# Kernel tuning notes

Measured on AMD Instinct MI355X. Metric: run time of the kernel, lower is better.

The kernel has to match this reference:

```python
import jax, jax.numpy as jnp
import numpy as np

HEADS = 2
OUT_CH = 128
NEG_SLOPE_ATT = 0.2   # GATv2Conv attention LeakyReLU
NEG_SLOPE_ACT = 0.01  # nn.LeakyReLU default
BN_EPS = 1e-5


def setup_inputs() -> dict:
    key = jax.random.key(0)
    ks = jax.random.split(key, 8)
    B, C, D, H, W = 2, 128, 8, 32, 32
    N = B * D * H * W            # 16384 graph nodes
    E = 196608                   # avg degree 12
    x = jax.random.normal(ks[0], (B, C, D, H, W), dtype=jnp.float32)
    edge_index = jax.random.randint(ks[1], (2, E), 0, N, dtype=jnp.int64)
    lin_w = jax.random.normal(ks[2], (C, HEADS * OUT_CH), dtype=jnp.float32) * (1.0 / np.sqrt(C))
    lin_b = jax.random.normal(ks[3], (HEADS * OUT_CH,), dtype=jnp.float32) * 0.02
    att = jax.random.normal(ks[4], (HEADS, OUT_CH), dtype=jnp.float32) * (1.0 / np.sqrt(OUT_CH))
    gat_bias = jax.random.normal(ks[5], (OUT_CH,), dtype=jnp.float32) * 0.02
    bn_gamma = jnp.ones((OUT_CH,), dtype=jnp.float32)
    bn_beta = jnp.zeros((OUT_CH,), dtype=jnp.float32)
    return {"x": x, "edge_index": edge_index, "lin_w": lin_w, "lin_b": lin_b,
            "att": att, "gat_bias": gat_bias, "bn_gamma": bn_gamma, "bn_beta": bn_beta}


def _gatv2(xf, src, dst, lin_w, lin_b, att, gat_bias, n_nodes):
    # shared-weights GATv2: x' = x W + b, per edge e=(j->i): score = a . lrelu(x'_i + x'_j)
    h = (xf @ lin_w + lin_b).reshape(n_nodes, HEADS, OUT_CH)  # [N, H, C]
    x_src = h[src]                                            # [E, H, C] messages
    logits = jnp.einsum('ehc,hc->eh', jax.nn.leaky_relu(x_src + h[dst], NEG_SLOPE_ATT), att)
    # segment softmax over edges sharing the same target node
    m = jax.ops.segment_max(logits, dst, num_segments=n_nodes)      # [N, H]
    ex = jnp.exp(logits - m[dst])
    denom = jax.ops.segment_sum(ex, dst, num_segments=n_nodes)      # [N, H]
    alpha = ex / denom[dst]
    out = jax.ops.segment_sum(x_src * alpha[..., None], dst, num_segments=n_nodes)  # [N, H, C]
    return out.mean(axis=1) + gat_bias  # concat=False -> head mean


def reference(x, edge_index, lin_w, lin_b, att, gat_bias, bn_gamma, bn_beta):
    B, C, D, H, W = x.shape
    N = B * D * H * W
    xf = x.reshape(B, C, -1).transpose(0, 2, 1).reshape(N, C)
    # add_self_loops=True (PyG default)
    loop = jnp.arange(N, dtype=edge_index.dtype)
    src = jnp.concatenate([edge_index[0], loop])
    dst = jnp.concatenate([edge_index[1], loop])
    out = _gatv2(xf, src, dst, lin_w, lin_b, att, gat_bias, N)      # [N, OUT_CH]
    out = out.reshape(B, D * H * W, OUT_CH).transpose(0, 2, 1).reshape(B, OUT_CH, D, H, W)
    # BatchNorm3d (training-mode batch stats, biased variance)
    mean = out.mean(axis=(0, 2, 3, 4), keepdims=True)
    var = out.var(axis=(0, 2, 3, 4), keepdims=True)
    out = (out - mean) / jnp.sqrt(var + BN_EPS)
    out = out * bn_gamma.reshape(1, -1, 1, 1, 1) + bn_beta.reshape(1, -1, 1, 1, 1)
    return jax.nn.leaky_relu(out, NEG_SLOPE_ACT)
```

## Files before the change

### kernel.cpp

```cpp
#include <hip/hip_runtime.h>
#include <math.h>

#define N_NODES 16384
#define CIN 128
#define HOUT 256
#define OUTC 128
#define NEG_ATT 0.2f
#define NEG_ACT 0.01f
#define BN_EPS 1e-5f

static __device__ __forceinline__ unsigned short f2bf(float f) {
    unsigned int u = __float_as_uint(f);
    unsigned int r = (u + 0x7FFFu + ((u >> 16) & 1u)) >> 16;
    return (unsigned short)r;
}
static __device__ __forceinline__ float bf2f(unsigned short s) {
    return __uint_as_float(((unsigned int)s) << 16);
}

__global__ __launch_bounds__(256) void gemm_kernel(const float* __restrict__ x,
                                                   const float* __restrict__ lin_w,
                                                   const float* __restrict__ lin_b,
                                                   unsigned short* __restrict__ h) {
    __shared__ float As[32][64];
    __shared__ float Bs[32][64];
    const int t = threadIdx.x;
    const int n0 = blockIdx.y * 64;
    const int o0 = blockIdx.x * 64;
    const int b = n0 >> 13;
    const int s0 = n0 & 8191;
    const int tx = t & 15;
    const int ty = t >> 4;
    float acc[4][4] = {};

    const int col = t & 63;
    const int r0 = t >> 6;

    for (int kk = 0; kk < CIN; kk += 32) {
#pragma unroll
        for (int kr = 0; kr < 32; kr += 4) {
            int k = kk + kr + r0;
            As[kr + r0][col] = x[((b * CIN + k) << 13) + s0 + col];
            Bs[kr + r0][col] = lin_w[k * HOUT + o0 + col];
        }
        __syncthreads();
#pragma unroll
        for (int k = 0; k < 32; k++) {
            float4 av = ((const float4*)(&As[k][0]))[ty];
            float4 bv = ((const float4*)(&Bs[k][0]))[tx];
            float a[4] = {av.x, av.y, av.z, av.w};
            float bb[4] = {bv.x, bv.y, bv.z, bv.w};
#pragma unroll
            for (int i = 0; i < 4; i++)
#pragma unroll
                for (int j = 0; j < 4; j++)
                    acc[i][j] = fmaf(a[i], bb[j], acc[i][j]);
        }
        __syncthreads();
    }
    float4 lb = *(const float4*)(&lin_b[o0 + tx * 4]);
#pragma unroll
    for (int i = 0; i < 4; i++) {
        int n = n0 + ty * 4 + i;
        ushort4 o;
        o.x = f2bf(acc[i][0] + lb.x);
        o.y = f2bf(acc[i][1] + lb.y);
        o.z = f2bf(acc[i][2] + lb.z);
        o.w = f2bf(acc[i][3] + lb.w);
        ((ushort4*)h)[n * 64 + (o0 >> 2) + tx] = o;
    }
}

__global__ void count_kernel(const int* __restrict__ dst, int* __restrict__ deg, int E) {
    int e = blockIdx.x * 256 + threadIdx.x;
    if (e < E) atomicAdd(&deg[dst[e]], 1);
}

__global__ __launch_bounds__(1024) void scan_kernel(const int* __restrict__ deg,
                                                    int* __restrict__ row_ptr,
                                                    int* __restrict__ cursor) {
    __shared__ int sums[1024];
    const int t = threadIdx.x;
    int local[16];
    int s = 0;
#pragma unroll
    for (int k = 0; k < 16; k++) {
        local[k] = deg[t * 16 + k];
        s += local[k];
    }
    sums[t] = s;
    __syncthreads();
    for (int off = 1; off < 1024; off <<= 1) {
        int v = (t >= off) ? sums[t - off] : 0;
        __syncthreads();
        sums[t] += v;
        __syncthreads();
    }
    int run = sums[t] - s;
#pragma unroll
    for (int k = 0; k < 16; k++) {
        row_ptr[t * 16 + k] = run;
        cursor[t * 16 + k] = run;
        run += local[k];
    }
    if (t == 1023) row_ptr[N_NODES] = run;
}

__global__ void scatter_kernel(const int* __restrict__ edges, int* __restrict__ cursor,
                               int* __restrict__ csr, int E) {
    int e = blockIdx.x * 256 + threadIdx.x;
    if (e < E) {
        int s = edges[e];
        int d = edges[E + e];
        int p = atomicAdd(&cursor[d], 1);
        csr[p] = s;
    }
}

__global__ __launch_bounds__(256) void gat_kernel(const unsigned short* __restrict__ h,
                                                  const int* __restrict__ row_ptr,
                                                  const int* __restrict__ csr,
                                                  const float* __restrict__ att,
                                                  const float* __restrict__ gat_bias,
                                                  float* __restrict__ gat) {
    const int t = threadIdx.x;
    const int lane = t & 63;
    const int node = (blockIdx.x << 2) + (t >> 6);
    const ushort4* __restrict__ h4 = (const ushort4*)h;

    ushort4 hd4 = h4[(node << 6) + lane];
    float hdx = bf2f(hd4.x), hdy = bf2f(hd4.y), hdz = bf2f(hd4.z), hdw = bf2f(hd4.w);
    float4 a4 = ((const float4*)att)[lane];
    float m = -INFINITY, denom = 0.0f;
    float4 acc = make_float4(0.f, 0.f, 0.f, 0.f);

    const int beg = row_ptr[node];
    const int end = row_ptr[node + 1];
    const int cnt = end - beg + 1;

    for (int base = 0; base < cnt; base += 4) {
        int j[4];
#pragma unroll
        for (int u = 0; u < 4; u++) {
            int e = base + u;
            j[u] = (e == 0 || e >= cnt) ? node : csr[beg + e - 1];
        }
        float4 hj[4];
        float p[4];
#pragma unroll
        for (int u = 0; u < 4; u++) {
            ushort4 hv = h4[(j[u] << 6) + lane];
            hj[u].x = bf2f(hv.x); hj[u].y = bf2f(hv.y);
            hj[u].z = bf2f(hv.z); hj[u].w = bf2f(hv.w);
            float vx = hj[u].x + hdx; vx = vx > 0.f ? vx : NEG_ATT * vx;
            float vy = hj[u].y + hdy; vy = vy > 0.f ? vy : NEG_ATT * vy;
            float vz = hj[u].z + hdz; vz = vz > 0.f ? vz : NEG_ATT * vz;
            float vw = hj[u].w + hdw; vw = vw > 0.f ? vw : NEG_ATT * vw;
            p[u] = vx * a4.x + vy * a4.y + vz * a4.z + vw * a4.w;
        }
#pragma unroll
        for (int s = 1; s <= 16; s <<= 1) {
#pragma unroll
            for (int u = 0; u < 4; u++) p[u] += __shfl_xor(p[u], s);
        }
#pragma unroll
        for (int u = 0; u < 4; u++)
            if (base + u >= cnt) p[u] = -INFINITY;
        float nm = m;
#pragma unroll
        for (int u = 0; u < 4; u++) nm = fmaxf(nm, p[u]);
        float scale = __expf(m - nm);
        float w[4];
#pragma unroll
        for (int u = 0; u < 4; u++) w[u] = __expf(p[u] - nm);
        denom = denom * scale + w[0] + w[1] + w[2] + w[3];
        acc.x = acc.x * scale + w[0] * hj[0].x + w[1] * hj[1].x + w[2] * hj[2].x + w[3] * hj[3].x;
        acc.y = acc.y * scale + w[0] * hj[0].y + w[1] * hj[1].y + w[2] * hj[2].y + w[3] * hj[3].y;
        acc.z = acc.z * scale + w[0] * hj[0].z + w[1] * hj[1].z + w[2] * hj[2].z + w[3] * hj[3].z;
        acc.w = acc.w * scale + w[0] * hj[0].w + w[1] * hj[1].w + w[2] * hj[2].w + w[3] * hj[3].w;
        m = nm;
    }
    float inv = 1.0f / denom;
    float rx = acc.x * inv, ry = acc.y * inv, rz = acc.z * inv, rw = acc.w * inv;
    rx += __shfl_xor(rx, 32);
    ry += __shfl_xor(ry, 32);
    rz += __shfl_xor(rz, 32);
    rw += __shfl_xor(rw, 32);
    if (lane < 32) {
        float4 gb = ((const float4*)gat_bias)[lane];
        float4 o;
        o.x = 0.5f * rx + gb.x;
        o.y = 0.5f * ry + gb.y;
        o.z = 0.5f * rz + gb.z;
        o.w = 0.5f * rw + gb.w;
        ((float4*)gat)[(node << 5) + lane] = o;
    }
}

__global__ __launch_bounds__(256) void bn_reduce(const float* __restrict__ gat,
                                                 float* __restrict__ gsum,
                                                 float* __restrict__ gsumsq, int total) {
    __shared__ float ssum[256], ssq[256];
    const int t = threadIdx.x;
    float s = 0.f, q = 0.f;
    for (int i = blockIdx.x * 256 + t; i < total; i += 256 * gridDim.x) {
        float v = gat[i];
        s += v;
        q += v * v;
    }
    ssum[t] = s;
    ssq[t] = q;
    __syncthreads();
    if (t < 128) {
        atomicAdd(&gsum[t], ssum[t] + ssum[t + 128]);
        atomicAdd(&gsumsq[t], ssq[t] + ssq[t + 128]);
    }
}

__global__ __launch_bounds__(256) void epilogue_kernel(const float* __restrict__ gat,
                                                       const float* __restrict__ gsum,
                                                       const float* __restrict__ gsumsq,
                                                       const float* __restrict__ gamma,
                                                       const float* __restrict__ beta,
                                                       float* __restrict__ out) {
    __shared__ float tile[64 * 129];
    __shared__ float sc[128], sh[128];
    const int t = threadIdx.x;
    if (t < 128) {
        const float invN = 1.0f / (float)N_NODES;
        float mean = gsum[t] * invN;
        float var = gsumsq[t] * invN - mean * mean;
        float rstd = rsqrtf(var + BN_EPS);
        float s = gamma[t] * rstd;
        sc[t] = s;
        sh[t] = beta[t] - mean * s;
    }
    __syncthreads();
    const int n0 = blockIdx.x * 64;
    const int b = n0 >> 13;
    const int s0 = n0 & 8191;
#pragma unroll
    for (int k = 0; k < 32; k++) {
        int f = t + k * 256;
        int nl = f >> 7;
        int c = f & 127;
        float v = gat[(n0 << 7) + f];
        v = v * sc[c] + sh[c];
        v = v > 0.f ? v : NEG_ACT * v;
        tile[nl * 129 + c] = v;
    }
    __syncthreads();
    const int sl = t & 63;
    const int c0 = t >> 6;
#pragma unroll
    for (int k = 0; k < 32; k++) {
        int c = c0 + (k << 2);
        out[((b * OUTC + c) << 13) + s0 + sl] = tile[sl * 129 + c];
    }
}

extern "C" void kernel_launch(void* const* d_in, const int* in_sizes, int n_in,
                              void* d_out, int out_size, void* d_ws, size_t ws_size,
                              hipStream_t stream) {
    const float* x        = (const float*)d_in[0];
    const int*   edges    = (const int*)d_in[1];
    const float* lin_w    = (const float*)d_in[2];
    const float* lin_b    = (const float*)d_in[3];
    const float* att      = (const float*)d_in[4];
    const float* gat_bias = (const float*)d_in[5];
    const float* bn_gamma = (const float*)d_in[6];
    const float* bn_beta  = (const float*)d_in[7];
    float* out = (float*)d_out;
    const int E = in_sizes[1] / 2;

    char* ws = (char*)d_ws;
    unsigned short* h = (unsigned short*)(ws);
    float* gat     = (float*)(ws + 8388608);
    int*   deg     = (int*)(ws + 16777216);
    int*   row_ptr = (int*)(ws + 16842752);
    int*   cursor  = (int*)(ws + 16912384);
    int*   csr     = (int*)(ws + 16977920);
    float* gsum    = (float*)(ws + 17764352);
    float* gsumsq  = gsum + 128;

    hipMemsetAsync(deg, 0, N_NODES * sizeof(int), stream);
    hipMemsetAsync(gsum, 0, 256 * sizeof(float), stream);

    gemm_kernel<<<dim3(HOUT / 64, N_NODES / 64), 256, 0, stream>>>(x, lin_w, lin_b, h);
    count_kernel<<<(E + 255) / 256, 256, 0, stream>>>(edges + E, deg, E);
    scan_kernel<<<1, 1024, 0, stream>>>(deg, row_ptr, cursor);
    scatter_kernel<<<(E + 255) / 256, 256, 0, stream>>>(edges, cursor, csr, E);
    gat_kernel<<<N_NODES / 4, 256, 0, stream>>>(h, row_ptr, csr, att, gat_bias, gat);
    bn_reduce<<<256, 256, 0, stream>>>(gat, gsum, gsumsq, N_NODES * OUTC);
    epilogue_kernel<<<N_NODES / 64, 256, 0, stream>>>(gat, gsum, gsumsq, bn_gamma, bn_beta, out);
}
```

Measured before the change: 167.5 us.

## Use bf16 MFMA GEMM, fuse CSR build into cooperative kernel, fuse BN stats

Replaces the scalar FP32 GEMM with a bf16 MFMA 16x16x32 GEMM that stages bf16 tiles in LDS and also zeroes the degree and stat buffers, removing the memsets. The count/scan/scatter kernels become one cooperative kernel with grid syncs, and the BN reduction is folded into the GAT kernel through shared and global atomics. The GAT kernel now handles 4 nodes per wave and unrolls 8 edges per iteration. These changes cut launches and a full re-read of the GAT output, at the cost of bf16 rounding of inputs, cooperative-launch constraints and atomic float ordering nondeterminism.

```diff
diff --git a/kernel.cpp b/kernel.cpp
--- a/kernel.cpp
+++ b/kernel.cpp
@@ -1,5 +1,8 @@
 #include <hip/hip_runtime.h>
+#include <hip/hip_cooperative_groups.h>
 #include <math.h>
+
+namespace cg = cooperative_groups;
 
 #define N_NODES 16384
 #define CIN 128
@@ -9,6 +12,9 @@
 #define NEG_ACT 0.01f
 #define BN_EPS 1e-5f
 
+typedef short short8 __attribute__((ext_vector_type(8)));
+typedef float f32x4 __attribute__((ext_vector_type(4)));
+
 static __device__ __forceinline__ unsigned short f2bf(float f) {
     unsigned int u = __float_as_uint(f);
     unsigned int r = (u + 0x7FFFu + ((u >> 16) & 1u)) >> 16;
@@ -18,102 +24,135 @@
     return __uint_as_float(((unsigned int)s) << 16);
 }
 
+#define LDP 136
 __global__ __launch_bounds__(256) void gemm_kernel(const float* __restrict__ x,
                                                    const float* __restrict__ lin_w,
                                                    const float* __restrict__ lin_b,
-                                                   unsigned short* __restrict__ h) {
-    __shared__ float As[32][64];
-    __shared__ float Bs[32][64];
+                                                   unsigned short* __restrict__ h,
+                                                   int* __restrict__ deg,
+                                                   float* __restrict__ gz) {
+    __shared__ __align__(16) unsigned short A_s[64 * LDP];
+    __shared__ __align__(16) unsigned short Bt_s[64 * LDP];
     const int t = threadIdx.x;
-    const int n0 = blockIdx.y * 64;
-    const int o0 = blockIdx.x * 64;
-    const int b = n0 >> 13;
-    const int s0 = n0 & 8191;
-    const int tx = t & 15;
-    const int ty = t >> 4;
-    float acc[4][4] = {};
-
-    const int col = t & 63;
-    const int r0 = t >> 6;
-
-    for (int kk = 0; kk < CIN; kk += 32) {
-#pragma unroll
-        for (int kr = 0; kr < 32; kr += 4) {
-            int k = kk + kr + r0;
-            As[kr + r0][col] = x[((b * CIN + k) << 13) + s0 + col];
-            Bs[kr + r0][col] = lin_w[k * HOUT + o0 + col];
-        }
-        __syncthreads();
-#pragma unroll
-        for (int k = 0; k < 32; k++) {
-            float4 av = ((const float4*)(&As[k][0]))[ty];
-            float4 bv = ((const float4*)(&Bs[k][0]))[tx];
-            float a[4] = {av.x, av.y, av.z, av.w};
-            float bb[4] = {bv.x, bv.y, bv.z, bv.w};
-#pragma unroll
-            for (int i = 0; i < 4; i++)
-#pragma unroll
-                for (int j = 0; j < 4; j++)
-                    acc[i][j] = fmaf(a[i], bb[j], acc[i][j]);
-        }
-        __syncthreads();
-    }
-    float4 lb = *(const float4*)(&lin_b[o0 + tx * 4]);
-#pragma unroll
-    for (int i = 0; i < 4; i++) {
-        int n = n0 + ty * 4 + i;
-        ushort4 o;
-        o.x = f2bf(acc[i][0] + lb.x);
-        o.y = f2bf(acc[i][1] + lb.y);
-        o.z = f2bf(acc[i][2] + lb.z);
-        o.w = f2bf(acc[i][3] + lb.w);
-        ((ushort4*)h)[n * 64 + (o0 >> 2) + tx] = o;
-    }
-}
-
-__global__ void count_kernel(const int* __restrict__ dst, int* __restrict__ deg, int E) {
-    int e = blockIdx.x * 256 + threadIdx.x;
-    if (e < E) atomicAdd(&deg[dst[e]], 1);
-}
-
-__global__ __launch_bounds__(1024) void scan_kernel(const int* __restrict__ deg,
-                                                    int* __restrict__ row_ptr,
-                                                    int* __restrict__ cursor) {
-    __shared__ int sums[1024];
+    const int bid = blockIdx.x;
+
+    if (t < 16) deg[bid * 16 + t] = 0;
+    if (bid == 0) gz[t] = 0.f;
+
+    const int node0 = (bid >> 2) * 64;
+    const int o0 = (bid & 3) * 64;
+    const int b = node0 >> 13;
+    const int s0 = node0 & 8191;
+
+    const int nt = t & 15;
+    const int kt = t >> 4;
+#pragma unroll
+    for (int p = 0; p < 2; p++) {
+        const int kb = p * 64 + kt * 4;
+        float4 ar[4], br[4];
+#pragma unroll
+        for (int r = 0; r < 4; r++) {
+            ar[r] = *(const float4*)&x[((b * CIN + kb + r) << 13) + s0 + nt * 4];
+            br[r] = *(const float4*)&lin_w[(kb + r) * HOUT + o0 + nt * 4];
+        }
+#pragma unroll
+        for (int j = 0; j < 4; j++) {
+            ushort4 va, vb;
+            va.x = f2bf(((const float*)&ar[0])[j]);
+            va.y = f2bf(((const float*)&ar[1])[j]);
+            va.z = f2bf(((const float*)&ar[2])[j]);
+            va.w = f2bf(((const float*)&ar[3])[j]);
+            vb.x = f2bf(((const float*)&br[0])[j]);
+            vb.y = f2bf(((const float*)&br[1])[j]);
+            vb.z = f2bf(((const float*)&br[2])[j]);
+            vb.w = f2bf(((const float*)&br[3])[j]);
+            *(ushort4*)&A_s[(nt * 4 + j) * LDP + kb] = va;
+            *(ushort4*)&Bt_s[(nt * 4 + j) * LDP + kb] = vb;
+        }
+    }
+    __syncthreads();
+
+    const int w = t >> 6;
+    const int lane = t & 63;
+    const int lrow = lane & 15;
+    const int lquad = lane >> 4;
+    const int m0 = w * 16;
+
+    short8 afr[4];
+#pragma unroll
+    for (int ks = 0; ks < 4; ks++)
+        afr[ks] = *(const short8*)&A_s[(m0 + lrow) * LDP + ks * 32 + lquad * 8];
+
+    f32x4 acc[4];
+#pragma unroll
+    for (int c = 0; c < 4; c++) { acc[c][0] = 0.f; acc[c][1] = 0.f; acc[c][2] = 0.f; acc[c][3] = 0.f; }
+
+#pragma unroll
+    for (int c = 0; c < 4; c++) {
+#pragma unroll
+        for (int ks = 0; ks < 4; ks++) {
+            short8 bfr = *(const short8*)&Bt_s[(c * 16 + lrow) * LDP + ks * 32 + lquad * 8];
+            acc[c] = __builtin_amdgcn_mfma_f32_16x16x32_bf16(afr[ks], bfr, acc[c], 0, 0, 0);
+        }
+    }
+
+#pragma unroll
+    for (int c = 0; c < 4; c++) {
+        const int col = o0 + c * 16 + lrow;
+        const float lb = lin_b[col];
+#pragma unroll
+        for (int r = 0; r < 4; r++) {
+            const int n = node0 + m0 + lquad * 4 + r;
+            h[n * HOUT + col] = f2bf(acc[c][r] + lb);
+        }
+    }
+}
+
+__global__ __launch_bounds__(256) void csr_kernel(const int* __restrict__ edges, int E,
+                                                  int* __restrict__ deg,
+                                                  int* __restrict__ row_ptr,
+                                                  int* __restrict__ cursor,
+                                                  int* __restrict__ csr,
+                                                  int* __restrict__ partial) {
+    cg::grid_group grid = cg::this_grid();
     const int t = threadIdx.x;
-    int local[16];
-    int s = 0;
-#pragma unroll
-    for (int k = 0; k < 16; k++) {
-        local[k] = deg[t * 16 + k];
-        s += local[k];
-    }
-    sums[t] = s;
-    __syncthreads();
-    for (int off = 1; off < 1024; off <<= 1) {
-        int v = (t >= off) ? sums[t - off] : 0;
-        __syncthreads();
-        sums[t] += v;
-        __syncthreads();
-    }
-    int run = sums[t] - s;
-#pragma unroll
-    for (int k = 0; k < 16; k++) {
-        row_ptr[t * 16 + k] = run;
-        cursor[t * 16 + k] = run;
-        run += local[k];
-    }
-    if (t == 1023) row_ptr[N_NODES] = run;
-}
-
-__global__ void scatter_kernel(const int* __restrict__ edges, int* __restrict__ cursor,
-                               int* __restrict__ csr, int E) {
-    int e = blockIdx.x * 256 + threadIdx.x;
-    if (e < E) {
-        int s = edges[e];
+    const int bid = blockIdx.x;
+    __shared__ int excl_s[64];
+
+    for (int e = bid * 256 + t; e < E; e += 256 * 256)
+        atomicAdd(&deg[edges[E + e]], 1);
+    grid.sync();
+
+    if (t < 64) {
+        int d = deg[bid * 64 + t];
+        int v = d;
+#pragma unroll
+        for (int off = 1; off < 64; off <<= 1) {
+            int u = __shfl_up(v, off);
+            if (t >= off) v += u;
+        }
+        excl_s[t] = v - d;
+        if (t == 63) partial[bid] = v;
+    }
+    grid.sync();
+
+    if (t < 64) {
+        int s = 0;
+        for (int j = t; j < bid; j += 64) s += partial[j];
+#pragma unroll
+        for (int off = 1; off < 64; off <<= 1) s += __shfl_xor(s, off);
+        int rp = s + excl_s[t];
+        row_ptr[bid * 64 + t] = rp;
+        cursor[bid * 64 + t] = rp;
+        if (bid == 255 && t == 63) row_ptr[N_NODES] = s + excl_s[63] + deg[N_NODES - 1];
+    }
+    grid.sync();
+
+    for (int e = bid * 256 + t; e < E; e += 256 * 256) {
+        int src = edges[e];
         int d = edges[E + e];
         int p = atomicAdd(&cursor[d], 1);
-        csr[p] = s;
+        csr[p] = src;
     }
 }
 
@@ -122,98 +161,110 @@
                                                   const int* __restrict__ csr,
                                                   const float* __restrict__ att,
                                                   const float* __restrict__ gat_bias,
-                                                  float* __restrict__ gat) {
+                                                  float* __restrict__ gat,
+                                                  float* __restrict__ gsum,
+                                                  float* __restrict__ gsumsq) {
     const int t = threadIdx.x;
     const int lane = t & 63;
-    const int node = (blockIdx.x << 2) + (t >> 6);
+    const int w = t >> 6;
+    __shared__ float ssum[128], ssq[128];
+    if (t < 128) { ssum[t] = 0.f; ssq[t] = 0.f; }
+    __syncthreads();
+
     const ushort4* __restrict__ h4 = (const ushort4*)h;
-
-    ushort4 hd4 = h4[(node << 6) + lane];
-    float hdx = bf2f(hd4.x), hdy = bf2f(hd4.y), hdz = bf2f(hd4.z), hdw = bf2f(hd4.w);
     float4 a4 = ((const float4*)att)[lane];
-    float m = -INFINITY, denom = 0.0f;
-    float4 acc = make_float4(0.f, 0.f, 0.f, 0.f);
-
-    const int beg = row_ptr[node];
-    const int end = row_ptr[node + 1];
-    const int cnt = end - beg + 1;
-
-    for (int base = 0; base < cnt; base += 4) {
-        int j[4];
-#pragma unroll
-        for (int u = 0; u < 4; u++) {
-            int e = base + u;
-            j[u] = (e == 0 || e >= cnt) ? node : csr[beg + e - 1];
-        }
-        float4 hj[4];
-        float p[4];
-#pragma unroll
-        for (int u = 0; u < 4; u++) {
-            ushort4 hv = h4[(j[u] << 6) + lane];
-            hj[u].x = bf2f(hv.x); hj[u].y = bf2f(hv.y);
-            hj[u].z = bf2f(hv.z); hj[u].w = bf2f(hv.w);
-            float vx = hj[u].x + hdx; vx = vx > 0.f ? vx : NEG_ATT * vx;
-            float vy = hj[u].y + hdy; vy = vy > 0.f ? vy : NEG_ATT * vy;
-            float vz = hj[u].z + hdz; vz = vz > 0.f ? vz : NEG_ATT * vz;
-            float vw = hj[u].w + hdw; vw = vw > 0.f ? vw : NEG_ATT * vw;
-            p[u] = vx * a4.x + vy * a4.y + vz * a4.z + vw * a4.w;
-        }
-#pragma unroll
-        for (int s = 1; s <= 16; s <<= 1) {
-#pragma unroll
-            for (int u = 0; u < 4; u++) p[u] += __shfl_xor(p[u], s);
-        }
-#pragma unroll
-        for (int u = 0; u < 4; u++)
-            if (base + u >= cnt) p[u] = -INFINITY;
-        float nm = m;
-#pragma unroll
-        for (int u = 0; u < 4; u++) nm = fmaxf(nm, p[u]);
-        float scale = __expf(m - nm);
-        float w[4];
-#pragma unroll
-        for (int u = 0; u < 4; u++) w[u] = __expf(p[u] - nm);
-        denom = denom * scale + w[0] + w[1] + w[2] + w[3];
-        acc.x = acc.x * scale + w[0] * hj[0].x + w[1] * hj[1].x + w[2] * hj[2].x + w[3] * hj[3].x;
-        acc.y = acc.y * scale + w[0] * hj[0].y + w[1] * hj[1].y + w[2] * hj[2].y + w[3] * hj[3].y;
-        acc.z = acc.z * scale + w[0] * hj[0].z + w[1] * hj[1].z + w[2] * hj[2].z + w[3] * hj[3].z;
-        acc.w = acc.w * scale + w[0] * hj[0].w + w[1] * hj[1].w + w[2] * hj[2].w + w[3] * hj[3].w;
-        m = nm;
-    }
-    float inv = 1.0f / denom;
-    float rx = acc.x * inv, ry = acc.y * inv, rz = acc.z * inv, rw = acc.w * inv;
-    rx += __shfl_xor(rx, 32);
-    ry += __shfl_xor(ry, 32);
-    rz += __shfl_xor(rz, 32);
-    rw += __shfl_xor(rw, 32);
+    float4 gb = ((const float4*)gat_bias)[lane & 31];
+    float st[4] = {0.f, 0.f, 0.f, 0.f}, sq[4] = {0.f, 0.f, 0.f, 0.f};
+
+    for (int i = 0; i < 4; i++) {
+        const int node = (blockIdx.x << 4) + (w << 2) + i;
+        ushort4 hd4 = h4[(node << 6) + lane];
+        float hdx = bf2f(hd4.x), hdy = bf2f(hd4.y), hdz = bf2f(hd4.z), hdw = bf2f(hd4.w);
+        const int beg = row_ptr[node];
+        const int cnt = row_ptr[node + 1] - beg + 1;
+        float m = -INFINITY, denom = 0.f;
+        float4 acc = make_float4(0.f, 0.f, 0.f, 0.f);
+
+        for (int base = 0; base < cnt; base += 8) {
+            int j[8];
+#pragma unroll
+            for (int u = 0; u < 8; u++) {
+                int e = base + u;
+                j[u] = (e == 0 || e >= cnt) ? node : csr[beg + e - 1];
+            }
+            float4 hj[8];
+            float p[8];
+#pragma unroll
+            for (int u = 0; u < 8; u++) {
+                ushort4 hv = h4[(j[u] << 6) + lane];
+                hj[u].x = bf2f(hv.x); hj[u].y = bf2f(hv.y);
+                hj[u].z = bf2f(hv.z); hj[u].w = bf2f(hv.w);
+                float vx = hj[u].x + hdx; vx = vx > 0.f ? vx : NEG_ATT * vx;
+                float vy = hj[u].y + hdy; vy = vy > 0.f ? vy : NEG_ATT * vy;
+                float vz = hj[u].z + hdz; vz = vz > 0.f ? vz : NEG_ATT * vz;
+                float vw = hj[u].w + hdw; vw = vw > 0.f ? vw : NEG_ATT * vw;
+                p[u] = vx * a4.x + vy * a4.y + vz * a4.z + vw * a4.w;
+            }
+#pragma unroll
+            for (int s = 1; s <= 16; s <<= 1) {
+#pragma unroll
+                for (int u = 0; u < 8; u++) p[u] += __shfl_xor(p[u], s);
+            }
+#pragma unroll
+            for (int u = 0; u < 8; u++)
+                if (base + u >= cnt) p[u] = -INFINITY;
+            float nm = m;
+#pragma unroll
+            for (int u = 0; u < 8; u++) nm = fmaxf(nm, p[u]);
+            float scale = __expf(m - nm);
+            float wt[8];
+#pragma unroll
+            for (int u = 0; u < 8; u++) wt[u] = __expf(p[u] - nm);
+            float wsum = 0.f;
+#pragma unroll
+            for (int u = 0; u < 8; u++) wsum += wt[u];
+            denom = denom * scale + wsum;
+            float ax = acc.x * scale, ay = acc.y * scale, az = acc.z * scale, aw = acc.w * scale;
+#pragma unroll
+            for (int u = 0; u < 8; u++) {
+                ax = fmaf(wt[u], hj[u].x, ax);
+                ay = fmaf(wt[u], hj[u].y, ay);
+                az = fmaf(wt[u], hj[u].z, az);
+                aw = fmaf(wt[u], hj[u].w, aw);
+            }
+            acc.x = ax; acc.y = ay; acc.z = az; acc.w = aw;
+            m = nm;
+        }
+        float inv = 1.0f / denom;
+        float rx = acc.x * inv, ry = acc.y * inv, rz = acc.z * inv, rw = acc.w * inv;
+        rx += __shfl_xor(rx, 32);
+        ry += __shfl_xor(ry, 32);
+        rz += __shfl_xor(rz, 32);
+        rw += __shfl_xor(rw, 32);
+        if (lane < 32) {
+            float4 o;
+            o.x = 0.5f * rx + gb.x;
+            o.y = 0.5f * ry + gb.y;
+            o.z = 0.5f * rz + gb.z;
+            o.w = 0.5f * rw + gb.w;
+            ((float4*)gat)[(node << 5) + lane] = o;
+            st[0] += o.x; sq[0] += o.x * o.x;
+            st[1] += o.y; sq[1] += o.y * o.y;
+            st[2] += o.z; sq[2] += o.z * o.z;
+            st[3] += o.w; sq[3] += o.w * o.w;
+        }
+    }
     if (lane < 32) {
-        float4 gb = ((const float4*)gat_bias)[lane];
-        float4 o;
-        o.x = 0.5f * rx + gb.x;
-        o.y = 0.5f * ry + gb.y;
-        o.z = 0.5f * rz + gb.z;
-        o.w = 0.5f * rw + gb.w;
-        ((float4*)gat)[(node << 5) + lane] = o;
-    }
-}
-
-__global__ __launch_bounds__(256) void bn_reduce(const float* __restrict__ gat,
-                                                 float* __restrict__ gsum,
-                                                 float* __restrict__ gsumsq, int total) {
-    __shared__ float ssum[256], ssq[256];
-    const int t = threadIdx.x;
-    float s = 0.f, q = 0.f;
-    for (int i = blockIdx.x * 256 + t; i < total; i += 256 * gridDim.x) {
-        float v = gat[i];
-        s += v;
-        q += v * v;
-    }
-    ssum[t] = s;
-    ssq[t] = q;
+#pragma unroll
+        for (int c = 0; c < 4; c++) {
+            atomicAdd(&ssum[(lane << 2) + c], st[c]);
+            atomicAdd(&ssq[(lane << 2) + c], sq[c]);
+        }
+    }
     __syncthreads();
     if (t < 128) {
-        atomicAdd(&gsum[t], ssum[t] + ssum[t + 128]);
-        atomicAdd(&gsumsq[t], ssq[t] + ssq[t + 128]);
+        atomicAdd(&gsum[t], ssum[t]);
+        atomicAdd(&gsumsq[t], ssq[t]);
     }
 }
 
@@ -271,26 +322,28 @@
     const float* bn_gamma = (const float*)d_in[6];
     const float* bn_beta  = (const float*)d_in[7];
     float* out = (float*)d_out;
-    const int E = in_sizes[1] / 2;
+    int E = in_sizes[1] / 2;
 
     char* ws = (char*)d_ws;
     unsigned short* h = (unsigned short*)(ws);
     float* gat     = (float*)(ws + 8388608);
     int*   deg     = (int*)(ws + 16777216);
     int*   row_ptr = (int*)(ws + 16842752);
-    int*   cursor  = (int*)(ws + 16912384);
-    int*   csr     = (int*)(ws + 16977920);
-    float* gsum    = (float*)(ws + 17764352);
+    int*   cursor  = (int*)(ws + 16908544);
+    int*   csr     = (int*)(ws + 16974080);
+    int*   partial = (int*)(ws + 17825792);
+    float* gsum    = (float*)(ws + 17827840);
     float* gsumsq  = gsum + 128;
 
-    hipMemsetAsync(deg, 0, N_NODES * sizeof(int), stream);
-    hipMemsetAsync(gsum, 0, 256 * sizeof(float), stream);
-
-    gemm_kernel<<<dim3(HOUT / 64, N_NODES / 64), 256, 0, stream>>>(x, lin_w, lin_b, h);
-    count_kernel<<<(E + 255) / 256, 256, 0, stream>>>(edges + E, deg, E);
-    scan_kernel<<<1, 1024, 0, stream>>>(deg, row_ptr, cursor);
-    scatter_kernel<<<(E + 255) / 256, 256, 0, stream>>>(edges, cursor, csr, E);
-    gat_kernel<<<N_NODES / 4, 256, 0, stream>>>(h, row_ptr, csr, att, gat_bias, gat);
-    bn_reduce<<<256, 256, 0, stream>>>(gat, gsum, gsumsq, N_NODES * OUTC);
+    gemm_kernel<<<1024, 256, 0, stream>>>(x, lin_w, lin_b, h, deg, gsum);
+
+    const int* edges_a = edges;
+    int E_a = E;
+    int* deg_a = deg; int* row_ptr_a = row_ptr; int* cursor_a = cursor;
+    int* csr_a = csr; int* partial_a = partial;
+    void* cargs[] = {&edges_a, &E_a, &deg_a, &row_ptr_a, &cursor_a, &csr_a, &partial_a};
+    hipLaunchCooperativeKernel((void*)csr_kernel, dim3(256), dim3(256), cargs, 0, stream);
+
+    gat_kernel<<<N_NODES / 16, 256, 0, stream>>>(h, row_ptr, csr, att, gat_bias, gat, gsum, gsumsq);
     epilogue_kernel<<<N_NODES / 64, 256, 0, stream>>>(gat, gsum, gsumsq, bn_gamma, bn_beta, out);
 }
```

New measurement: 262.5 us. +56.7%, slower.
